# Performance work log

Hardware: AMD Instinct MI355X
Metric: run time of the kernel (lower is better)

The kernel has to match this reference:

```python
import jax, jax.numpy as jnp
import numpy as np

NB, H = 4, 16
EPS = 1e-5


def _ln(x, w=None, b=None):
    m = jnp.mean(x, -1, keepdims=True)
    v = jnp.var(x, -1, keepdims=True)
    y = (x - m) * jax.lax.rsqrt(v + EPS)
    if w is not None:
        y = y * w
    if b is not None:
        y = y + b
    return y


def _ada_ln(a, s, ln_s_w, w_gamma, w_beta):
    # AF3 Algorithm 26: a <- sigmoid(Lin(LN_nobias(s))) * LN_noaffine(a) + Lin(LN_nobias(s))
    a_n = _ln(a)
    s_n = _ln(s, ln_s_w)
    return jax.nn.sigmoid(s_n @ w_gamma) * a_n + s_n @ w_beta


def setup_inputs():
    key = jax.random.key(0)
    B, S, c_a, c_s, c_z = 1, 1024, 768, 384, 128
    n_hidden = 2 * c_a  # expansion factor n=2
    ks = iter(jax.random.split(key, 40))

    def rn(shape, scale=1.0):
        return scale * jax.random.normal(next(ks), shape, dtype=jnp.float32)

    p = 0.02
    return {
        "a": rn((B, S, c_a)),
        "s": rn((B, S, c_s)),
        "z": rn((B, S, S, c_z)),
        "beta": rn((B, S, S, H)),
        # per-block AttentionPairBias params (stacked over NB blocks)
        "ln_s_w_attn": jnp.ones((NB, c_s)),
        "wg_attn": rn((NB, c_s, c_a), p),
        "wb_attn": rn((NB, c_s, c_a), p),
        "wq": rn((NB, c_a, c_a), p),
        "bq": jnp.zeros((NB, c_a)),
        "wk": rn((NB, c_a, c_a), p),
        "wv": rn((NB, c_a, c_a), p),
        "ln_z_w": jnp.ones((NB, c_z)),
        "ln_z_b": jnp.zeros((NB, c_z)),
        "wpb": rn((NB, c_z, H), p),
        "wgate": rn((NB, c_a, c_a), p),
        "wo": rn((NB, c_a, c_a), p),
        "wsg_attn": rn((NB, c_s, c_a), p),
        "bsg_attn": -2.0 * jnp.ones((NB, c_a)),
        # per-block ConditionedTransitionBlock params
        "ln_s_w_tr": jnp.ones((NB, c_s)),
        "wg_tr": rn((NB, c_s, c_a), p),
        "wb_tr": rn((NB, c_s, c_a), p),
        "w_swish": rn((NB, c_a, n_hidden), p),
        "w_gate2": rn((NB, c_a, n_hidden), p),
        "wsg_tr": rn((NB, c_s, c_a), p),
        "bsg_tr": -2.0 * jnp.ones((NB, c_a)),
        "w_out": rn((NB, n_hidden, c_a), p),
    }


def reference(a, s, z, beta, ln_s_w_attn, wg_attn, wb_attn, wq, bq, wk, wv,
              ln_z_w, ln_z_b, wpb, wgate, wo, wsg_attn, bsg_attn,
              ln_s_w_tr, wg_tr, wb_tr, w_swish, w_gate2, wsg_tr, bsg_tr, w_out):
    B, S, c_a = a.shape
    d = c_a // H
    scale = 1.0 / jnp.sqrt(jnp.float32(d))
    for i in range(NB):
        # --- AttentionPairBias (AF3 Alg 24) ---
        ah = _ada_ln(a, s, ln_s_w_attn[i], wg_attn[i], wb_attn[i])
        q = (ah @ wq[i] + bq[i]).reshape(B, S, H, d)
        k = (ah @ wk[i]).reshape(B, S, H, d)
        v = (ah @ wv[i]).reshape(B, S, H, d)
        zb = _ln(z, ln_z_w[i], ln_z_b[i]) @ wpb[i]  # [B,S,S,H] pair bias
        scores = jnp.einsum('bihd,bjhd->bhij', q, k) * scale \
                 + jnp.transpose(zb + beta, (0, 3, 1, 2))
        attn = jax.nn.softmax(scores, axis=-1)
        o = jnp.einsum('bhij,bjhd->bihd', attn, v)
        g = jax.nn.sigmoid(ah @ wgate[i]).reshape(B, S, H, d)
        att_out = (g * o).reshape(B, S, c_a) @ wo[i]
        b_attn = jax.nn.sigmoid(s @ wsg_attn[i] + bsg_attn[i]) * att_out
        # --- ConditionedTransitionBlock (AF3 Alg 25, SwiGLU) ---
        th = _ada_ln(a, s, ln_s_w_tr[i], wg_tr[i], wb_tr[i])
        hidden = jax.nn.silu(th @ w_swish[i]) * (th @ w_gate2[i])
        tr = jax.nn.sigmoid(s @ wsg_tr[i] + bsg_tr[i]) * (hidden @ w_out[i])
        a = b_attn + tr
    return a
```

## Files before the change

### kernel.cpp

```cpp
#include <hip/hip_runtime.h>
#include <hip/hip_bf16.h>

typedef __hip_bfloat16 bf16;
typedef __attribute__((ext_vector_type(8))) short s8v;
typedef __attribute__((ext_vector_type(4))) float f4v;

constexpr int S = 1024, CA = 768, CS = 384, CZ = 128, NHID = 1536;
constexpr int NBLK = 4, NHEAD = 16, DH = 48;
constexpr float EPS = 1e-5f;

#define DEV static __device__ __forceinline__

DEV float sigmoidf_(float x) { return 1.0f / (1.0f + __expf(-x)); }

DEV f4v mfma16(s8v a, s8v b, f4v c) {
  return __builtin_amdgcn_mfma_f32_16x16x32_bf16(a, b, c, 0, 0, 0);
}

union U8 { s8v s; bf16 h[8]; };
union U4 { uint2 u; bf16 h[4]; };

DEV float wred_sum(float v) {
#pragma unroll
  for (int o = 32; o; o >>= 1) v += __shfl_xor(v, o);
  return v;
}

struct PrepFatArgs {
  const float* tsrc[14];
  bf16* tdst[14];
  const float* tcs[14];
  long tdstZ[14];
  const float *ln_z_w, *ln_z_b, *wpb, *bq, *bsg_a, *bsg_t;
  bf16* W2T; float* bias2; float* biasQKVG; float* biasSG;
  const float* s_in; bf16* s_hat; bf16* s_bf;
};

__global__ __launch_bounds__(256) void prep_fat(PrepFatArgs a) {
  __shared__ __align__(16) float tile[1056];
  const int bid = blockIdx.x, t = threadIdx.x;
  if (bid < 32256) {
    int ti, blk, x, y, K, N;
    if (bid < 6912) {
      const int lb = bid; ti = lb / 1152; const int r2 = lb % 1152;
      blk = r2 / 288; const int rem = r2 % 288; x = rem % 24; y = rem / 24; K = 384; N = 768;
    } else if (bid < 18432) {
      const int lb = bid - 6912; ti = 6 + lb / 2304; const int r2 = lb % 2304;
      blk = r2 / 576; const int rem = r2 % 576; x = rem % 24; y = rem / 24; K = 768; N = 768;
    } else if (bid < 27648) {
      const int lb = bid - 18432; ti = 11 + lb / 4608; const int r2 = lb % 4608;
      blk = r2 / 1152; const int rem = r2 % 1152; x = rem % 48; y = rem / 48; K = 768; N = 1536;
    } else {
      const int lb = bid - 27648; ti = 13; blk = lb / 1152;
      const int rem = lb % 1152; x = rem % 24; y = rem / 24; K = 1536; N = 768;
    }
    const float* src = a.tsrc[ti] + (size_t)blk * K * N;
    bf16* dst = a.tdst[ti] + (size_t)blk * a.tdstZ[ti];
    const float* cs = a.tcs[ti] ? (a.tcs[ti] + blk * CS) : nullptr;
    const int k0 = y * 32, n0 = x * 32, tx = t & 31, ty = t >> 5;
#pragma unroll
    for (int q = 0; q < 4; ++q) {
      const int k = k0 + ty + 8 * q;
      float v = src[(size_t)k * N + n0 + tx];
      if (cs) v *= cs[k];
      tile[(ty + 8 * q) * 33 + tx] = v;
    }
    __syncthreads();
#pragma unroll
    for (int q = 0; q < 4; ++q)
      dst[(size_t)(n0 + ty + 8 * q) * K + k0 + tx] = __float2bfloat16(tile[tx * 33 + ty + 8 * q]);
    return;
  }
  if (bid < 32305) {
    const int pid = bid - 32256;
    if (pid == 48) {
      for (int f = t; f < 64 * CZ; f += 256) {
        const int col = f >> 7, c = f & 127, b = col >> 4, h = col & 15;
        a.W2T[f] = __float2bfloat16(a.ln_z_w[b * CZ + c] * a.wpb[(b * CZ + c) * NHEAD + h]);
      }
      if (t < 64) {
        const int b = t >> 4, h = t & 15;
        float sum = 0.f;
        for (int c = 0; c < CZ; ++c)
          sum += a.ln_z_b[b * CZ + c] * a.wpb[(b * CZ + c) * NHEAD + h];
        a.bias2[t] = sum;
      }
      return;
    }
    const int g = pid * 256 + t;
    if (g < 4 * 3072) {
      const int b = g / 3072, c = g % 3072;
      a.biasQKVG[g] = (c < 768) ? a.bq[b * 768 + c] : 0.f;
    }
    if (g < 6144) {
      const int b = g / 1536, c = g % 1536;
      a.biasSG[g] = (c < 768) ? a.bsg_a[b * 768 + c] : a.bsg_t[b * 768 + c - 768];
    }
    return;
  }
  {
    float* red = tile;
    const size_t row = bid - 32305;
    float4 v = make_float4(0.f, 0.f, 0.f, 0.f);
    if (t < CS / 4) v = ((const float4*)(a.s_in + row * CS))[t];
    float sum = v.x + v.y + v.z + v.w;
    float sq = v.x * v.x + v.y * v.y + v.z * v.z + v.w * v.w;
    sum = wred_sum(sum); sq = wred_sum(sq);
    const int wv = t >> 6;
    if ((t & 63) == 0) { red[2 * wv] = sum; red[2 * wv + 1] = sq; }
    __syncthreads();
    sum = red[0] + red[2] + red[4] + red[6];
    sq = red[1] + red[3] + red[5] + red[7];
    const float m = sum / CS;
    const float rstd = rsqrtf(sq / CS - m * m + EPS);
    if (t < CS / 4) {
      U4 oh, ob_;
      oh.h[0] = __float2bfloat16((v.x - m) * rstd); oh.h[1] = __float2bfloat16((v.y - m) * rstd);
      oh.h[2] = __float2bfloat16((v.z - m) * rstd); oh.h[3] = __float2bfloat16((v.w - m) * rstd);
      ob_.h[0] = __float2bfloat16(v.x); ob_.h[1] = __float2bfloat16(v.y);
      ob_.h[2] = __float2bfloat16(v.z); ob_.h[3] = __float2bfloat16(v.w);
      *(uint2*)(a.s_hat + row * CS + 4 * t) = oh.u;
      *(uint2*)(a.s_bf + row * CS + 4 * t) = ob_.u;
    }
  }
}

__global__ __launch_bounds__(256) void ln_adaln2(const float* __restrict__ a,
                                                 const bf16* __restrict__ ada,
                                                 bf16* __restrict__ ah_attn,
                                                 bf16* __restrict__ ah_tr) {
  __shared__ float red[8];
  const int t = threadIdx.x;
  const size_t row = blockIdx.x;
  float4 v = make_float4(0.f, 0.f, 0.f, 0.f);
  if (t < 192) v = ((const float4*)(a + row * CA))[t];
  float sum = v.x + v.y + v.z + v.w;
  float sq = v.x * v.x + v.y * v.y + v.z * v.z + v.w * v.w;
  sum = wred_sum(sum); sq = wred_sum(sq);
  const int wv = t >> 6;
  if ((t & 63) == 0) { red[2 * wv] = sum; red[2 * wv + 1] = sq; }
  __syncthreads();
  sum = red[0] + red[2] + red[4] + red[6];
  sq = red[1] + red[3] + red[5] + red[7];
  const float m = sum / CA;
  const float rstd = rsqrtf(sq / CA - m * m + EPS);
  if (t < 192) {
    const float an[4] = {(v.x - m) * rstd, (v.y - m) * rstd, (v.z - m) * rstd, (v.w - m) * rstd};
    const bf16* ar = ada + row * 12288 + 4 * t;
    U4 g1, b1, g2, b2, o1, o2;
    g1.u = *(const uint2*)(ar);
    b1.u = *(const uint2*)(ar + 768);
    g2.u = *(const uint2*)(ar + 1536);
    b2.u = *(const uint2*)(ar + 2304);
#pragma unroll
    for (int j = 0; j < 4; ++j) {
      o1.h[j] = __float2bfloat16(sigmoidf_(__bfloat162float(g1.h[j])) * an[j] + __bfloat162float(b1.h[j]));
      o2.h[j] = __float2bfloat16(sigmoidf_(__bfloat162float(g2.h[j])) * an[j] + __bfloat162float(b2.h[j]));
    }
    *(uint2*)(ah_attn + row * CA + 4 * t) = o1.u;
    *(uint2*)(ah_tr + row * CA + 4 * t) = o2.u;
  }
}

__global__ __launch_bounds__(256) void final_adaln(const float* __restrict__ sg,
                                                   const bf16* __restrict__ att,
                                                   const bf16* __restrict__ tr,
                                                   const bf16* __restrict__ ada,
                                                   bf16* __restrict__ ah_attn,
                                                   bf16* __restrict__ ah_tr) {
  __shared__ float red[8];
  const int t = threadIdx.x;
  const size_t row = blockIdx.x;
  float o[4] = {0.f, 0.f, 0.f, 0.f};
  if (t < 192) {
    const float4 sa = *(const float4*)(sg + row * 6144 + 4 * t);
    const float4 st = *(const float4*)(sg + row * 6144 + 768 + 4 * t);
    U4 av, tv;
    av.u = *(const uint2*)(att + row * CA + 4 * t);
    tv.u = *(const uint2*)(tr + row * CA + 4 * t);
    o[0] = sa.x * __bfloat162float(av.h[0]) + st.x * __bfloat162float(tv.h[0]);
    o[1] = sa.y * __bfloat162float(av.h[1]) + st.y * __bfloat162float(tv.h[1]);
    o[2] = sa.z * __bfloat162float(av.h[2]) + st.z * __bfloat162float(tv.h[2]);
    o[3] = sa.w * __bfloat162float(av.h[3]) + st.w * __bfloat162float(tv.h[3]);
  }
  float sum = o[0] + o[1] + o[2] + o[3];
  float sq = o[0] * o[0] + o[1] * o[1] + o[2] * o[2] + o[3] * o[3];
  sum = wred_sum(sum); sq = wred_sum(sq);
  const int wv = t >> 6;
  if ((t & 63) == 0) { red[2 * wv] = sum; red[2 * wv + 1] = sq; }
  __syncthreads();
  sum = red[0] + red[2] + red[4] + red[6];
  sq = red[1] + red[3] + red[5] + red[7];
  const float m = sum / CA;
  const float rstd = rsqrtf(sq / CA - m * m + EPS);
  if (t < 192) {
    const bf16* ar = ada + row * 12288 + 4 * t;
    U4 g1, b1, g2, b2, o1, o2;
    g1.u = *(const uint2*)(ar);
    b1.u = *(const uint2*)(ar + 768);
    g2.u = *(const uint2*)(ar + 1536);
    b2.u = *(const uint2*)(ar + 2304);
#pragma unroll
    for (int j = 0; j < 4; ++j) {
      const float an = (o[j] - m) * rstd;
      o1.h[j] = __float2bfloat16(sigmoidf_(__bfloat162float(g1.h[j])) * an + __bfloat162float(b1.h[j]));
      o2.h[j] = __float2bfloat16(sigmoidf_(__bfloat162float(g2.h[j])) * an + __bfloat162float(b2.h[j]));
    }
    *(uint2*)(ah_attn + row * CA + 4 * t) = o1.u;
    *(uint2*)(ah_tr + row * CA + 4 * t) = o2.u;
  }
}

__global__ __launch_bounds__(256) void ew_final(const float* __restrict__ sg,
                                                const bf16* __restrict__ att,
                                                const bf16* __restrict__ tr,
                                                float* __restrict__ out) {
  const int i = blockIdx.x * 256 + threadIdx.x;
  const int row = i / 192, col = (i % 192) * 4;
  const float4 sa = *(const float4*)(sg + (size_t)row * 6144 + col);
  const float4 st = *(const float4*)(sg + (size_t)row * 6144 + 768 + col);
  U4 av, tv;
  av.u = *(const uint2*)(att + (size_t)row * CA + col);
  tv.u = *(const uint2*)(tr + (size_t)row * CA + col);
  float4 o;
  o.x = sa.x * __bfloat162float(av.h[0]) + st.x * __bfloat162float(tv.h[0]);
  o.y = sa.y * __bfloat162float(av.h[1]) + st.y * __bfloat162float(tv.h[1]);
  o.z = sa.z * __bfloat162float(av.h[2]) + st.z * __bfloat162float(tv.h[2]);
  o.w = sa.w * __bfloat162float(av.h[3]) + st.w * __bfloat162float(tv.h[3]);
  *(float4*)(out + (size_t)row * CA + col) = o;
}

__global__ __launch_bounds__(256) void zbias_kernel(const float* __restrict__ z,
                                                    const float* __restrict__ beta,
                                                    const bf16* __restrict__ W2T,
                                                    const float* __restrict__ bias2,
                                                    bf16* __restrict__ bias_all) {
  __shared__ s8v zt8[64 * 16];
  __shared__ s8v w2s[64 * 16];
  __shared__ float betas[64][17];
  __shared__ float bias2s[64];
  __shared__ bf16 obuf[64][72];
  const int t = threadIdx.x;
  const int i = blockIdx.y, j0 = blockIdx.x * 64;
#pragma unroll
  for (int q = 0; q < 4; ++q) {
    const int u = q * 256 + t;
    const int row = u >> 4, sl = u & 15;
    w2s[row * 16 + (sl ^ (row & 7))] = *(const s8v*)(W2T + row * CZ + sl * 8);
  }
  if (t < 64) bias2s[t] = bias2[t];
  {
    const int j = t >> 2, h4 = t & 3;
    const float4 bv = *(const float4*)(beta + ((size_t)i * S + j0 + j) * NHEAD + 4 * h4);
    betas[j][4 * h4 + 0] = bv.x; betas[j][4 * h4 + 1] = bv.y;
    betas[j][4 * h4 + 2] = bv.z; betas[j][4 * h4 + 3] = bv.w;
  }
  {
    const int p = t >> 2, q = t & 3;
    const float* zr = z + ((size_t)i * S + j0 + p) * CZ + q * 32;
    float vals[32];
    float sum = 0.f, sq = 0.f;
#pragma unroll
    for (int k4 = 0; k4 < 8; ++k4) {
      const float4 xv = *(const float4*)(zr + 4 * k4);
      vals[4 * k4 + 0] = xv.x; vals[4 * k4 + 1] = xv.y;
      vals[4 * k4 + 2] = xv.z; vals[4 * k4 + 3] = xv.w;
      sum += xv.x + xv.y + xv.z + xv.w;
      sq += xv.x * xv.x + xv.y * xv.y + xv.z * xv.z + xv.w * xv.w;
    }
    sum += __shfl_xor(sum, 1); sum += __shfl_xor(sum, 2);
    sq += __shfl_xor(sq, 1); sq += __shfl_xor(sq, 2);
    const float m = sum / CZ;
    const float rstd = rsqrtf(sq / CZ - m * m + EPS);
#pragma unroll
    for (int u = 0; u < 4; ++u) {
      U8 pk;
#pragma unroll
      for (int e = 0; e < 8; ++e) pk.h[e] = __float2bfloat16((vals[8 * u + e] - m) * rstd);
      const int cu = 4 * q + u;
      zt8[p * 16 + (cu ^ (p & 7))] = pk.s;
    }
  }
  __syncthreads();
  const int lane = t & 63, wid = t >> 6;
  const int wr = wid >> 1, wc = wid & 1;
  const int ln = lane & 15, lq = lane >> 4;
  f4v acc[2][2] = {};
#pragma unroll
  for (int kk = 0; kk < 4; ++kk) {
    const int sl = (lq + 4 * kk) ^ (ln & 7);
    s8v a[2], b[2];
#pragma unroll
    for (int mi = 0; mi < 2; ++mi) a[mi] = zt8[(32 * wr + 16 * mi + ln) * 16 + sl];
#pragma unroll
    for (int ni = 0; ni < 2; ++ni) b[ni] = w2s[(32 * wc + 16 * ni + ln) * 16 + sl];
#pragma unroll
    for (int mi = 0; mi < 2; ++mi)
#pragma unroll
      for (int ni = 0; ni < 2; ++ni) acc[mi][ni] = mfma16(a[mi], b[ni], acc[mi][ni]);
  }
#pragma unroll
  for (int mi = 0; mi < 2; ++mi)
#pragma unroll
    for (int ni = 0; ni < 2; ++ni) {
      const int col = 32 * wc + 16 * ni + ln;
      const int jb = 32 * wr + 16 * mi + 4 * lq;
      U4 o4;
#pragma unroll
      for (int r = 0; r < 4; ++r)
        o4.h[r] = __float2bfloat16(acc[mi][ni][r] + bias2s[col] + betas[jb + r][col & 15]);
      *(uint2*)&obuf[col][jb] = o4.u;
    }
  __syncthreads();
  {
    const int oc = t >> 2, js = (t & 3) * 16;
    bf16* dp = bias_all + (size_t)oc * S * S + (size_t)i * S + j0 + js;
    *(s8v*)dp = *(const s8v*)&obuf[oc][js];
    *(s8v*)(dp + 8) = *(const s8v*)&obuf[oc][js + 8];
  }
}

struct GemmAArgs {
  const bf16* A0[2]; int lda0[2];
  const bf16* A1[2]; int lda1[2];
  const bf16* Bt[2];
  const float* bias[2];
  void* C[2];
  int K[2]; int N[2]; int nb[2];
  int amode[2]; int outMode[2];
  bf16* vT;
  const float* opA;
  const float* mlA;
  const bf16* gateA;
};

DEV s8v combineRT(s8v x, s8v y, int amode) {
  U8 ux, uy, rr;
  ux.s = x; uy.s = y;
#pragma unroll
  for (int j = 0; j < 8; ++j) {
    const float fx = __bfloat162float(ux.h[j]);
    const float fy = __bfloat162float(uy.h[j]);
    const float tt = sigmoidf_(fx);
    rr.h[j] = __float2bfloat16((amode == 2 ? fx * tt : tt) * fy);
  }
  return rr.s;
}

DEV s8v combineFlash(const float* opart, const float* ml, const bf16* gate,
                     int row, int k) {
  const int h = k / DH;
  const float2 m1 = ((const float2*)ml)[(size_t)h * S + row];
  const float2 m2 = ((const float2*)ml)[(size_t)(NHEAD + h) * S + row];
  const float M = fmaxf(m1.x, m2.x);
  const float w1 = __expf(m1.x - M), w2 = __expf(m2.x - M);
  const float inv = 1.0f / (w1 * m1.y + w2 * m2.y);
  const float* o1p = opart + (size_t)row * CA + k;
  const float* o2p = opart + (size_t)S * CA + (size_t)row * CA + k;
  U8 g; g.s = *(const s8v*)(gate + (size_t)row * 3072 + k);
  U8 r;
#pragma unroll
  for (int j = 0; j < 8; ++j) {
    const float v = (w1 * o1p[j] + w2 * o2p[j]) * inv;
    r.h[j] = __float2bfloat16(sigmoidf_(__bfloat162float(g.h[j])) * v);
  }
  return r.s;
}

__global__ __launch_bounds__(256) void gemmA(GemmAArgs ga) {
  const int z = blockIdx.z;
  if ((int)blockIdx.x >= ga.nb[z]) return;
  __shared__ s8v As[512];
  __shared__ s8v Bs[1024];
  const bf16* A0 = ga.A0[z]; const int lda0 = ga.lda0[z];
  const bf16* A1 = ga.A1[z]; const int lda1 = ga.lda1[z];
  const bf16* Bt = ga.Bt[z];
  const float* bias = ga.bias[z];
  const int K = ga.K[z], N = ga.N[z], amode = ga.amode[z], om = ga.outMode[z];
  const int t = threadIdx.x;
  const int lane = t & 63, wid = t >> 6;
  const int wr = wid >> 1, wc = wid & 1;
  const int ln = lane & 15, lq = lane >> 4;
  const int m0 = blockIdx.y * 64, n0 = blockIdx.x * 128;
  int rowA[2], slA[2], swzA[2];
#pragma unroll
  for (int q = 0; q < 2; ++q) {
    const int u = q * 256 + t;
    rowA[q] = u >> 3; slA[q] = u & 7;
    swzA[q] = rowA[q] * 8 + (slA[q] ^ (rowA[q] & 7));
  }
  int rowB[4], slB[4], swzB[4];
#pragma unroll
  for (int q = 0; q < 4; ++q) {
    const int u = q * 256 + t;
    rowB[q] = u >> 3; slB[q] = u & 7;
    swzB[q] = rowB[q] * 8 + (slB[q] ^ (rowB[q] & 7));
  }
  f4v acc[2][4] = {};
  s8v ra[2], ra2[2], rb[4];
  if (amode != 3) {
#pragma unroll
    for (int q = 0; q < 2; ++q) {
      ra[q] = *(const s8v*)(A0 + (size_t)(m0 + rowA[q]) * lda0 + slA[q] * 8);
      if (amode != 0) ra2[q] = *(const s8v*)(A1 + (size_t)(m0 + rowA[q]) * lda1 + slA[q] * 8);
    }
  }
#pragma unroll
  for (int q = 0; q < 4; ++q)
    rb[q] = *(const s8v*)(Bt + (size_t)(n0 + rowB[q]) * K + slB[q] * 8);
  for (int ks = 0;;) {
    __syncthreads();
    if (amode == 3) {
#pragma unroll
      for (int q = 0; q < 2; ++q)
        As[swzA[q]] = combineFlash(ga.opA, ga.mlA, ga.gateA, m0 + rowA[q], ks + slA[q] * 8);
    } else {
#pragma unroll
      for (int q = 0; q < 2; ++q)
        As[swzA[q]] = (amode == 0) ? ra[q] : combineRT(ra[q], ra2[q], amode);
    }
#pragma unroll
    for (int q = 0; q < 4; ++q) Bs[swzB[q]] = rb[q];
    const int ksn = ks + 64;
    if (ksn < K) {
      if (amode != 3) {
#pragma unroll
        for (int q = 0; q < 2; ++q) {
          ra[q] = *(const s8v*)(A0 + (size_t)(m0 + rowA[q]) * lda0 + ksn + slA[q] * 8);
          if (amode != 0) ra2[q] = *(const s8v*)(A1 + (size_t)(m0 + rowA[q]) * lda1 + ksn + slA[q] * 8);
        }
      }
#pragma unroll
      for (int q = 0; q < 4; ++q)
        rb[q] = *(const s8v*)(Bt + (size_t)(n0 + rowB[q]) * K + ksn + slB[q] * 8);
    }
    __syncthreads();
#pragma unroll
    for (int kk = 0; kk < 2; ++kk) {
      const int sl = (lq + 4 * kk) ^ (ln & 7);
      s8v a[2], b[4];
#pragma unroll
      for (int mi = 0; mi < 2; ++mi) a[mi] = As[(32 * wr + 16 * mi + ln) * 8 + sl];
#pragma unroll
      for (int ni = 0; ni < 4; ++ni) b[ni] = Bs[(64 * wc + 16 * ni + ln) * 8 + sl];
#pragma unroll
      for (int mi = 0; mi < 2; ++mi)
#pragma unroll
        for (int ni = 0; ni < 4; ++ni) acc[mi][ni] = mfma16(a[mi], b[ni], acc[mi][ni]);
    }
    ks = ksn;
    if (ks >= K) break;
  }
  const bool vdiv = (ga.vT != nullptr) && (z == 0) && (n0 >= 1536) && (n0 < 2304);
#pragma unroll
  for (int ni = 0; ni < 4; ++ni) {
    const int n = n0 + 64 * wc + 16 * ni + ln;
    const float bv = bias ? bias[n] : 0.f;
#pragma unroll
    for (int mi = 0; mi < 2; ++mi) {
      const int mb = m0 + 32 * wr + 16 * mi + 4 * lq;
      if (vdiv) {
        U4 o4;
#pragma unroll
        for (int r = 0; r < 4; ++r) o4.h[r] = __float2bfloat16(acc[mi][ni][r] + bv);
        *(uint2*)(ga.vT + (size_t)(n - 1536) * S + mb) = o4.u;
      } else if (om == 0) {
        bf16* Cb = (bf16*)ga.C[z];
#pragma unroll
        for (int r = 0; r < 4; ++r)
          Cb[(size_t)(mb + r) * N + n] = __float2bfloat16(acc[mi][ni][r] + bv);
      } else {
        float* Cf = (float*)ga.C[z];
#pragma unroll
        for (int r = 0; r < 4; ++r)
          Cf[(size_t)(mb + r) * N + n] = sigmoidf_(acc[mi][ni][r] + bv);
      }
    }
  }
}

__global__ __launch_bounds__(256) void flash_split(const bf16* __restrict__ qkvg,
                                                   const bf16* __restrict__ vT,
                                                   const bf16* __restrict__ bias_all,
                                                   float* __restrict__ opart,
                                                   float* __restrict__ ml, int blk) {
  __shared__ s8v Qs[64 * 8];
  __shared__ s8v Ks[2][64 * 8];
  __shared__ s8v Vs[2][48 * 8];
  __shared__ s8v Bs[2][64 * 8];
  __shared__ bf16 PwB[4 * 1024];
  __shared__ float facL[4][16];
  const int t = threadIdx.x;
  const int lane = t & 63, w = t >> 6;
  const int ln = lane & 15, lq = lane >> 4;
  const int h = blockIdx.y, i0 = blockIdx.x * 64, half = blockIdx.z;
  const bf16* bp = bias_all + (size_t)(blk * NHEAD + h) * S * S;
  const float scale = 0.14433756729740643f;

#pragma unroll
  for (int uu = 0; uu < 2; ++uu) {
    const int u = t + 256 * uu, row = u >> 3, sl = u & 7;
    s8v qv{};
    if (sl < 6) qv = *(const s8v*)(qkvg + (size_t)(i0 + row) * 3072 + h * DH + sl * 8);
    Qs[row * 8 + (sl ^ (row & 7))] = qv;
  }

  s8v kr[2], br[2], vr0{}, vr1{};
  auto prefetch = [&](int jt) {
    const int j0 = jt * 64;
#pragma unroll
    for (int uu = 0; uu < 2; ++uu) {
      const int u = t + 256 * uu, row = u >> 3, sl = u & 7;
      s8v kv{};
      if (sl < 6) kv = *(const s8v*)(qkvg + (size_t)(j0 + row) * 3072 + 768 + h * DH + sl * 8);
      kr[uu] = kv;
      br[uu] = *(const s8v*)(bp + (size_t)(i0 + row) * S + j0 + sl * 8);
    }
    { const int d = t >> 3, sl = t & 7;
      vr0 = *(const s8v*)(vT + (size_t)(h * DH + d) * S + j0 + sl * 8); }
    if (t < 128) {
      const int u = 256 + t, d = u >> 3, sl = u & 7;
      vr1 = *(const s8v*)(vT + (size_t)(h * DH + d) * S + j0 + sl * 8);
    }
  };
  auto store_tiles = [&](int pb) {
#pragma unroll
    for (int uu = 0; uu < 2; ++uu) {
      const int u = t + 256 * uu, row = u >> 3, sl = u & 7;
      const int ph = row * 8 + (sl ^ (row & 7));
      Ks[pb][ph] = kr[uu];
      Bs[pb][ph] = br[uu];
    }
    { const int d = t >> 3, sl = t & 7;
      Vs[pb][d * 8 + (sl ^ (d & 7))] = vr0; }
    if (t < 128) {
      const int u = 256 + t, d = u >> 3, sl = u & 7;
      Vs[pb][d * 8 + (sl ^ (d & 7))] = vr1;
    }
  };

  float m_run = -3e30f, l_run = 0.f;
  f4v acc_o[3] = {};
  bf16* pw = PwB + w * 1024;

  prefetch(half * 8);
  for (int jt2 = 0; jt2 < 8; ++jt2) {
    const int pb = jt2 & 1;
    __syncthreads();
    store_tiles(pb);
    __syncthreads();
    if (jt2 < 7) prefetch(half * 8 + jt2 + 1);
    float p[4][4];
    float tmax = -3e30f;
    __builtin_amdgcn_s_setprio(1);
#pragma unroll
    for (int ja = 0; ja < 4; ++ja) {
      f4v accs = {};
#pragma unroll
      for (int ks2 = 0; ks2 < 2; ++ks2) {
        const int sl = (lq + 4 * ks2) ^ (ln & 7);
        const s8v a = Ks[pb][(16 * ja + ln) * 8 + sl];
        const s8v b = Qs[(16 * w + ln) * 8 + sl];
        accs = mfma16(a, b, accs);
      }
      const int jq = 4 * ja + lq;
      const int pu = jq >> 1;
      U4 bv;
      bv.u = *(const uint2*)((const bf16*)(&Bs[pb][0]) +
                             (((16 * w + ln) * 8 + (pu ^ (ln & 7))) * 8 + (jq & 1) * 4));
#pragma unroll
      for (int r = 0; r < 4; ++r) {
        p[ja][r] = accs[r] * scale + __bfloat162float(bv.h[r]);
        tmax = fmaxf(tmax, p[ja][r]);
      }
    }
    __builtin_amdgcn_s_setprio(0);
    tmax = fmaxf(tmax, __shfl_xor(tmax, 16));
    tmax = fmaxf(tmax, __shfl_xor(tmax, 32));
    const float m_new = fmaxf(m_run, tmax);
    const float fac = __expf(m_run - m_new);
    m_run = m_new;
    float psum = 0.f;
#pragma unroll
    for (int ja = 0; ja < 4; ++ja)
#pragma unroll
      for (int r = 0; r < 4; ++r) {
        p[ja][r] = __expf(p[ja][r] - m_new);
        psum += p[ja][r];
      }
    psum += __shfl_xor(psum, 16);
    psum += __shfl_xor(psum, 32);
    l_run = l_run * fac + psum;
    if (lq == 0) facL[w][ln] = fac;
#pragma unroll
    for (int ja = 0; ja < 4; ++ja) {
      const int ju = 4 * ja + lq;
      const int ph = ju ^ ((ln & 7) << 1);
      U4 pk;
#pragma unroll
      for (int r = 0; r < 4; ++r) pk.h[r] = __float2bfloat16(p[ja][r]);
      *(uint2*)(pw + ln * 64 + ph * 4) = pk.u;
    }
    asm volatile("s_waitcnt lgkmcnt(0)" ::: "memory");
    __builtin_amdgcn_sched_barrier(0);
    const float4 fv = *(const float4*)&facL[w][4 * lq];
#pragma unroll
    for (int ni = 0; ni < 3; ++ni) {
      acc_o[ni][0] *= fv.x; acc_o[ni][1] *= fv.y;
      acc_o[ni][2] *= fv.z; acc_o[ni][3] *= fv.w;
    }
    __builtin_amdgcn_s_setprio(1);
#pragma unroll
    for (int ks2 = 0; ks2 < 2; ++ks2) {
      const int pu0 = (2 * lq + 8 * ks2) ^ ((ln & 7) << 1);
      const s8v pa = *(const s8v*)(pw + ln * 64 + pu0 * 4);
      const int slv = (lq + 4 * ks2) ^ (ln & 7);
#pragma unroll
      for (int ni = 0; ni < 3; ++ni) {
        const s8v vb = Vs[pb][(16 * ni + ln) * 8 + slv];
        acc_o[ni] = mfma16(pa, vb, acc_o[ni]);
      }
    }
    __builtin_amdgcn_s_setprio(0);
  }
  if (lq == 0) {
    ((float2*)ml)[(size_t)(half * NHEAD + h) * S + i0 + 16 * w + ln] =
        make_float2(m_run, l_run);
  }
  float* op = opart + (size_t)half * S * CA;
#pragma unroll
  for (int ni = 0; ni < 3; ++ni)
#pragma unroll
    for (int r = 0; r < 4; ++r) {
      const int m = i0 + 16 * w + 4 * lq + r;
      op[(size_t)m * CA + h * DH + 16 * ni + ln] = acc_o[ni][r];
    }
}

__global__ void fill_kernel(float* p, int n, float v) {
  const int i = blockIdx.x * 256 + threadIdx.x;
  if (i < n) p[i] = v;
}

extern "C" void kernel_launch(void* const* d_in, const int* in_sizes, int n_in,
                              void* d_out, int out_size, void* d_ws, size_t ws_size,
                              hipStream_t stream) {
  (void)in_sizes; (void)n_in;
  const float* a_in = (const float*)d_in[0];
  const float* s_in = (const float*)d_in[1];
  const float* z_in = (const float*)d_in[2];
  const float* beta = (const float*)d_in[3];
  const float* ln_s_w_attn = (const float*)d_in[4];
  const float* wg_attn = (const float*)d_in[5];
  const float* wb_attn = (const float*)d_in[6];
  const float* wq = (const float*)d_in[7];
  const float* bq = (const float*)d_in[8];
  const float* wk = (const float*)d_in[9];
  const float* wv = (const float*)d_in[10];
  const float* ln_z_w = (const float*)d_in[11];
  const float* ln_z_b = (const float*)d_in[12];
  const float* wpb = (const float*)d_in[13];
  const float* wgate = (const float*)d_in[14];
  const float* wo = (const float*)d_in[15];
  const float* wsg_attn = (const float*)d_in[16];
  const float* bsg_attn = (const float*)d_in[17];
  const float* ln_s_w_tr = (const float*)d_in[18];
  const float* wg_tr = (const float*)d_in[19];
  const float* wb_tr = (const float*)d_in[20];
  const float* w_swish = (const float*)d_in[21];
  const float* w_gate2 = (const float*)d_in[22];
  const float* wsg_tr = (const float*)d_in[23];
  const float* bsg_tr = (const float*)d_in[24];
  const float* w_out = (const float*)d_in[25];

  char* wp = (char*)d_ws;
  size_t used = 0;
  auto alloc = [&](size_t bytes) -> void* {
    void* p = wp + used;
    used += (bytes + 255) & ~(size_t)255;
    return p;
  };
  bf16* bias_all = (bf16*)alloc((size_t)64 * S * S * 2);
  bf16* WT_ada = (bf16*)alloc((size_t)4 * 3072 * 384 * 2);
  bf16* WT_sg = (bf16*)alloc((size_t)4 * 1536 * 384 * 2);
  bf16* WT_qkvg = (bf16*)alloc((size_t)4 * 3072 * 768 * 2);
  bf16* WT_wo = (bf16*)alloc((size_t)4 * 768 * 768 * 2);
  bf16* WT_mlp = (bf16*)alloc((size_t)4 * 3072 * 768 * 2);
  bf16* WT_wout = (bf16*)alloc((size_t)4 * 768 * 1536 * 2);
  float* biasQKVG = (float*)alloc(4 * 3072 * 4);
  float* biasSG = (float*)alloc(6144 * 4);
  bf16* W2T = (bf16*)alloc(64 * 128 * 2);
  float* bias2 = (float*)alloc(64 * 4);
  bf16* ada_all = (bf16*)alloc((size_t)S * 12288 * 2);
  float* sg_all = (float*)alloc((size_t)S * 6144 * 4);
  bf16* s_hat = (bf16*)alloc((size_t)S * CS * 2);
  bf16* s_bf = (bf16*)alloc((size_t)S * CS * 2);
  bf16* ah_attn = (bf16*)alloc((size_t)S * CA * 2);
  bf16* ah_tr = (bf16*)alloc((size_t)S * CA * 2);
  bf16* qkvg = (bf16*)alloc((size_t)S * 3072 * 2);
  bf16* vT = (bf16*)alloc((size_t)CA * S * 2);
  bf16* att = (bf16*)alloc((size_t)S * CA * 2);
  bf16* swg = (bf16*)alloc((size_t)S * 3072 * 2);
  bf16* trout = (bf16*)alloc((size_t)S * CA * 2);
  float* opart = (float*)alloc((size_t)2 * S * CA * 4);
  float* ml = (float*)alloc((size_t)2 * NHEAD * S * 8);
  if (used > ws_size) {
    fill_kernel<<<(out_size + 255) / 256, 256, 0, stream>>>((float*)d_out, out_size, 12345.0f);
    return;
  }

  const dim3 B256(256);

  {
    PrepFatArgs pa{};
    pa.tsrc[0] = wg_attn;  pa.tdst[0] = WT_ada + (size_t)0 * 384;    pa.tcs[0] = ln_s_w_attn; pa.tdstZ[0] = 3072 * 384;
    pa.tsrc[1] = wb_attn;  pa.tdst[1] = WT_ada + (size_t)768 * 384;  pa.tcs[1] = ln_s_w_attn; pa.tdstZ[1] = 3072 * 384;
    pa.tsrc[2] = wg_tr;    pa.tdst[2] = WT_ada + (size_t)1536 * 384; pa.tcs[2] = ln_s_w_tr;   pa.tdstZ[2] = 3072 * 384;
    pa.tsrc[3] = wb_tr;    pa.tdst[3] = WT_ada + (size_t)2304 * 384; pa.tcs[3] = ln_s_w_tr;   pa.tdstZ[3] = 3072 * 384;
    pa.tsrc[4] = wsg_attn; pa.tdst[4] = WT_sg + (size_t)0 * 384;     pa.tcs[4] = nullptr;     pa.tdstZ[4] = 1536 * 384;
    pa.tsrc[5] = wsg_tr;   pa.tdst[5] = WT_sg + (size_t)768 * 384;   pa.tcs[5] = nullptr;     pa.tdstZ[5] = 1536 * 384;
    pa.tsrc[6] = wq;    pa.tdst[6] = WT_qkvg + (size_t)0 * 768;    pa.tdstZ[6] = 3072 * 768;
    pa.tsrc[7] = wk;    pa.tdst[7] = WT_qkvg + (size_t)768 * 768;  pa.tdstZ[7] = 3072 * 768;
    pa.tsrc[8] = wv;    pa.tdst[8] = WT_qkvg + (size_t)1536 * 768; pa.tdstZ[8] = 3072 * 768;
    pa.tsrc[9] = wgate; pa.tdst[9] = WT_qkvg + (size_t)2304 * 768; pa.tdstZ[9] = 3072 * 768;
    pa.tsrc[10] = wo;   pa.tdst[10] = WT_wo;                       pa.tdstZ[10] = 768 * 768;
    pa.tsrc[11] = w_swish; pa.tdst[11] = WT_mlp + (size_t)0 * 768;    pa.tdstZ[11] = 3072 * 768;
    pa.tsrc[12] = w_gate2; pa.tdst[12] = WT_mlp + (size_t)1536 * 768; pa.tdstZ[12] = 3072 * 768;
    pa.tsrc[13] = w_out; pa.tdst[13] = WT_wout; pa.tdstZ[13] = 768 * 1536;
    pa.ln_z_w = ln_z_w; pa.ln_z_b = ln_z_b; pa.wpb = wpb;
    pa.bq = bq; pa.bsg_a = bsg_attn; pa.bsg_t = bsg_tr;
    pa.W2T = W2T; pa.bias2 = bias2; pa.biasQKVG = biasQKVG; pa.biasSG = biasSG;
    pa.s_in = s_in; pa.s_hat = s_hat; pa.s_bf = s_bf;
    prep_fat<<<33329, B256, 0, stream>>>(pa);
  }

  zbias_kernel<<<dim3(16, 1024), B256, 0, stream>>>(z_in, beta, W2T, bias2, bias_all);

  {
    GemmAArgs ga{};
    ga.A0[0] = s_hat; ga.lda0[0] = 384; ga.Bt[0] = WT_ada; ga.bias[0] = nullptr;
    ga.C[0] = ada_all; ga.K[0] = 384; ga.N[0] = 12288; ga.nb[0] = 96;
    ga.amode[0] = 0; ga.outMode[0] = 0;
    ga.A0[1] = s_bf; ga.lda0[1] = 384; ga.Bt[1] = WT_sg; ga.bias[1] = biasSG;
    ga.C[1] = sg_all; ga.K[1] = 384; ga.N[1] = 6144; ga.nb[1] = 48;
    ga.amode[1] = 0; ga.outMode[1] = 1;
    ga.vT = nullptr;
    gemmA<<<dim3(96, 16, 2), B256, 0, stream>>>(ga);
  }

  ln_adaln2<<<S, B256, 0, stream>>>(a_in, ada_all, ah_attn, ah_tr);
  for (int b = 0; b < NBLK; ++b) {
    {
      GemmAArgs ga{};
      ga.A0[0] = ah_attn; ga.lda0[0] = 768; ga.Bt[0] = WT_qkvg + (size_t)b * 3072 * 768;
      ga.bias[0] = biasQKVG + b * 3072; ga.C[0] = qkvg; ga.K[0] = 768; ga.N[0] = 3072;
      ga.nb[0] = 24; ga.amode[0] = 0; ga.outMode[0] = 0;
      ga.A0[1] = ah_tr; ga.lda0[1] = 768; ga.Bt[1] = WT_mlp + (size_t)b * 3072 * 768;
      ga.bias[1] = nullptr; ga.C[1] = swg; ga.K[1] = 768; ga.N[1] = 3072;
      ga.nb[1] = 24; ga.amode[1] = 0; ga.outMode[1] = 0;
      ga.vT = vT;
      gemmA<<<dim3(24, 16, 2), B256, 0, stream>>>(ga);
    }
    flash_split<<<dim3(16, 16, 2), B256, 0, stream>>>(qkvg, vT, bias_all, opart, ml, b);
    {
      GemmAArgs ga{};
      ga.A0[0] = nullptr; ga.lda0[0] = 0;
      ga.Bt[0] = WT_wo + (size_t)b * 768 * 768; ga.bias[0] = nullptr;
      ga.C[0] = att; ga.K[0] = 768; ga.N[0] = 768; ga.nb[0] = 6;
      ga.amode[0] = 3; ga.outMode[0] = 0;
      ga.A0[1] = swg; ga.lda0[1] = 3072; ga.A1[1] = swg + 1536; ga.lda1[1] = 3072;
      ga.Bt[1] = WT_wout + (size_t)b * 768 * 1536; ga.bias[1] = nullptr;
      ga.C[1] = trout; ga.K[1] = 1536; ga.N[1] = 768; ga.nb[1] = 6;
      ga.amode[1] = 2; ga.outMode[1] = 0;
      ga.vT = nullptr;
      ga.opA = opart; ga.mlA = ml; ga.gateA = qkvg + 2304;
      gemmA<<<dim3(6, 16, 2), B256, 0, stream>>>(ga);
    }
    if (b < NBLK - 1) {
      final_adaln<<<S, B256, 0, stream>>>(sg_all + (size_t)b * 1536, att, trout,
                                          ada_all + (size_t)(b + 1) * 3072, ah_attn, ah_tr);
    } else {
      ew_final<<<768, B256, 0, stream>>>(sg_all + (size_t)b * 1536, att, trout, (float*)d_out);
    }
  }
}
```

Before: 542.3 us.

## Fuse attention-out and transition-out GEMMs with gated residual into one tail kernel

Replaces the two-branch gemmA launch (Wo projection and W_out projection written to bf16 buffers) plus the final_adaln/ew_final combine with a single gemm_tail kernel. Each block computes both GEMMs into separate accumulators over 64x64 tiles and applies the sigmoid gates in the epilogue, writing the fp32 residual directly. The next block's adaLN then reuses ln_adaln2 on that fp32 buffer. This removes the att/trout intermediate round trips and one launch per block, and keeps the pre-LN sum in fp32. In exchange, gemm_tail uses smaller tiles with no register prefetch, and each block runs a sequential K=768 loop followed by a K=1536 loop, which may reduce latency hiding and per-block efficiency.

```diff
diff --git a/kernel.cpp b/kernel.cpp
--- a/kernel.cpp
+++ b/kernel.cpp
@@ -162,74 +162,6 @@
   }
 }
 
-__global__ __launch_bounds__(256) void final_adaln(const float* __restrict__ sg,
-                                                   const bf16* __restrict__ att,
-                                                   const bf16* __restrict__ tr,
-                                                   const bf16* __restrict__ ada,
-                                                   bf16* __restrict__ ah_attn,
-                                                   bf16* __restrict__ ah_tr) {
-  __shared__ float red[8];
-  const int t = threadIdx.x;
-  const size_t row = blockIdx.x;
-  float o[4] = {0.f, 0.f, 0.f, 0.f};
-  if (t < 192) {
-    const float4 sa = *(const float4*)(sg + row * 6144 + 4 * t);
-    const float4 st = *(const float4*)(sg + row * 6144 + 768 + 4 * t);
-    U4 av, tv;
-    av.u = *(const uint2*)(att + row * CA + 4 * t);
-    tv.u = *(const uint2*)(tr + row * CA + 4 * t);
-    o[0] = sa.x * __bfloat162float(av.h[0]) + st.x * __bfloat162float(tv.h[0]);
-    o[1] = sa.y * __bfloat162float(av.h[1]) + st.y * __bfloat162float(tv.h[1]);
-    o[2] = sa.z * __bfloat162float(av.h[2]) + st.z * __bfloat162float(tv.h[2]);
-    o[3] = sa.w * __bfloat162float(av.h[3]) + st.w * __bfloat162float(tv.h[3]);
-  }
-  float sum = o[0] + o[1] + o[2] + o[3];
-  float sq = o[0] * o[0] + o[1] * o[1] + o[2] * o[2] + o[3] * o[3];
-  sum = wred_sum(sum); sq = wred_sum(sq);
-  const int wv = t >> 6;
-  if ((t & 63) == 0) { red[2 * wv] = sum; red[2 * wv + 1] = sq; }
-  __syncthreads();
-  sum = red[0] + red[2] + red[4] + red[6];
-  sq = red[1] + red[3] + red[5] + red[7];
-  const float m = sum / CA;
-  const float rstd = rsqrtf(sq / CA - m * m + EPS);
-  if (t < 192) {
-    const bf16* ar = ada + row * 12288 + 4 * t;
-    U4 g1, b1, g2, b2, o1, o2;
-    g1.u = *(const uint2*)(ar);
-    b1.u = *(const uint2*)(ar + 768);
-    g2.u = *(const uint2*)(ar + 1536);
-    b2.u = *(const uint2*)(ar + 2304);
-#pragma unroll
-    for (int j = 0; j < 4; ++j) {
-      const float an = (o[j] - m) * rstd;
-      o1.h[j] = __float2bfloat16(sigmoidf_(__bfloat162float(g1.h[j])) * an + __bfloat162float(b1.h[j]));
-      o2.h[j] = __float2bfloat16(sigmoidf_(__bfloat162float(g2.h[j])) * an + __bfloat162float(b2.h[j]));
-    }
-    *(uint2*)(ah_attn + row * CA + 4 * t) = o1.u;
-    *(uint2*)(ah_tr + row * CA + 4 * t) = o2.u;
-  }
-}
-
-__global__ __launch_bounds__(256) void ew_final(const float* __restrict__ sg,
-                                                const bf16* __restrict__ att,
-                                                const bf16* __restrict__ tr,
-                                                float* __restrict__ out) {
-  const int i = blockIdx.x * 256 + threadIdx.x;
-  const int row = i / 192, col = (i % 192) * 4;
-  const float4 sa = *(const float4*)(sg + (size_t)row * 6144 + col);
-  const float4 st = *(const float4*)(sg + (size_t)row * 6144 + 768 + col);
-  U4 av, tv;
-  av.u = *(const uint2*)(att + (size_t)row * CA + col);
-  tv.u = *(const uint2*)(tr + (size_t)row * CA + col);
-  float4 o;
-  o.x = sa.x * __bfloat162float(av.h[0]) + st.x * __bfloat162float(tv.h[0]);
-  o.y = sa.y * __bfloat162float(av.h[1]) + st.y * __bfloat162float(tv.h[1]);
-  o.z = sa.z * __bfloat162float(av.h[2]) + st.z * __bfloat162float(tv.h[2]);
-  o.w = sa.w * __bfloat162float(av.h[3]) + st.w * __bfloat162float(tv.h[3]);
-  *(float4*)(out + (size_t)row * CA + col) = o;
-}
-
 __global__ __launch_bounds__(256) void zbias_kernel(const float* __restrict__ z,
                                                     const float* __restrict__ beta,
                                                     const bf16* __restrict__ W2T,
@@ -320,20 +252,6 @@
   }
 }
 
-struct GemmAArgs {
-  const bf16* A0[2]; int lda0[2];
-  const bf16* A1[2]; int lda1[2];
-  const bf16* Bt[2];
-  const float* bias[2];
-  void* C[2];
-  int K[2]; int N[2]; int nb[2];
-  int amode[2]; int outMode[2];
-  bf16* vT;
-  const float* opA;
-  const float* mlA;
-  const bf16* gateA;
-};
-
 DEV s8v combineRT(s8v x, s8v y, int amode) {
   U8 ux, uy, rr;
   ux.s = x; uy.s = y;
@@ -367,16 +285,25 @@
   return r.s;
 }
 
+struct GemmAArgs {
+  const bf16* A0[2]; int lda0[2];
+  const bf16* Bt[2];
+  const float* bias[2];
+  void* C[2];
+  int K[2]; int N[2]; int nb[2];
+  int outMode[2];
+  bf16* vT;
+};
+
 __global__ __launch_bounds__(256) void gemmA(GemmAArgs ga) {
   const int z = blockIdx.z;
   if ((int)blockIdx.x >= ga.nb[z]) return;
   __shared__ s8v As[512];
   __shared__ s8v Bs[1024];
   const bf16* A0 = ga.A0[z]; const int lda0 = ga.lda0[z];
-  const bf16* A1 = ga.A1[z]; const int lda1 = ga.lda1[z];
   const bf16* Bt = ga.Bt[z];
   const float* bias = ga.bias[z];
-  const int K = ga.K[z], N = ga.N[z], amode = ga.amode[z], om = ga.outMode[z];
+  const int K = ga.K[z], N = ga.N[z], om = ga.outMode[z];
   const int t = threadIdx.x;
   const int lane = t & 63, wid = t >> 6;
   const int wr = wid >> 1, wc = wid & 1;
@@ -397,39 +324,24 @@
     swzB[q] = rowB[q] * 8 + (slB[q] ^ (rowB[q] & 7));
   }
   f4v acc[2][4] = {};
-  s8v ra[2], ra2[2], rb[4];
-  if (amode != 3) {
-#pragma unroll
-    for (int q = 0; q < 2; ++q) {
-      ra[q] = *(const s8v*)(A0 + (size_t)(m0 + rowA[q]) * lda0 + slA[q] * 8);
-      if (amode != 0) ra2[q] = *(const s8v*)(A1 + (size_t)(m0 + rowA[q]) * lda1 + slA[q] * 8);
-    }
-  }
+  s8v ra[2], rb[4];
+#pragma unroll
+  for (int q = 0; q < 2; ++q)
+    ra[q] = *(const s8v*)(A0 + (size_t)(m0 + rowA[q]) * lda0 + slA[q] * 8);
 #pragma unroll
   for (int q = 0; q < 4; ++q)
     rb[q] = *(const s8v*)(Bt + (size_t)(n0 + rowB[q]) * K + slB[q] * 8);
   for (int ks = 0;;) {
     __syncthreads();
-    if (amode == 3) {
-#pragma unroll
-      for (int q = 0; q < 2; ++q)
-        As[swzA[q]] = combineFlash(ga.opA, ga.mlA, ga.gateA, m0 + rowA[q], ks + slA[q] * 8);
-    } else {
-#pragma unroll
-      for (int q = 0; q < 2; ++q)
-        As[swzA[q]] = (amode == 0) ? ra[q] : combineRT(ra[q], ra2[q], amode);
-    }
+#pragma unroll
+    for (int q = 0; q < 2; ++q) As[swzA[q]] = ra[q];
 #pragma unroll
     for (int q = 0; q < 4; ++q) Bs[swzB[q]] = rb[q];
     const int ksn = ks + 64;
     if (ksn < K) {
-      if (amode != 3) {
-#pragma unroll
-        for (int q = 0; q < 2; ++q) {
-          ra[q] = *(const s8v*)(A0 + (size_t)(m0 + rowA[q]) * lda0 + ksn + slA[q] * 8);
-          if (amode != 0) ra2[q] = *(const s8v*)(A1 + (size_t)(m0 + rowA[q]) * lda1 + ksn + slA[q] * 8);
-        }
-      }
+#pragma unroll
+      for (int q = 0; q < 2; ++q)
+        ra[q] = *(const s8v*)(A0 + (size_t)(m0 + rowA[q]) * lda0 + ksn + slA[q] * 8);
 #pragma unroll
       for (int q = 0; q < 4; ++q)
         rb[q] = *(const s8v*)(Bt + (size_t)(n0 + rowB[q]) * K + ksn + slB[q] * 8);
@@ -474,6 +386,93 @@
 #pragma unroll
         for (int r = 0; r < 4; ++r)
           Cf[(size_t)(mb + r) * N + n] = sigmoidf_(acc[mi][ni][r] + bv);
+      }
+    }
+  }
+}
+
+struct GemmTailArgs {
+  const float* opA; const float* mlA; const bf16* gateA;
+  const bf16* swg;
+  const bf16* BtWo; const bf16* BtWout;
+  const float* sg;
+  float* out;
+};
+
+__global__ __launch_bounds__(256) void gemm_tail(GemmTailArgs ga) {
+  __shared__ s8v As[512];
+  __shared__ s8v Bs[512];
+  const int t = threadIdx.x;
+  const int lane = t & 63, wid = t >> 6;
+  const int wr = wid >> 1, wc = wid & 1;
+  const int ln = lane & 15, lq = lane >> 4;
+  const int m0 = blockIdx.y * 64, n0 = blockIdx.x * 64;
+  int rowS[2], slS[2], swz[2];
+#pragma unroll
+  for (int q = 0; q < 2; ++q) {
+    const int u = q * 256 + t;
+    rowS[q] = u >> 3; slS[q] = u & 7;
+    swz[q] = rowS[q] * 8 + (slS[q] ^ (rowS[q] & 7));
+  }
+  f4v acc1[2][2] = {}, acc2[2][2] = {};
+  for (int ks = 0; ks < 768; ks += 64) {
+    __syncthreads();
+#pragma unroll
+    for (int q = 0; q < 2; ++q) {
+      As[swz[q]] = combineFlash(ga.opA, ga.mlA, ga.gateA, m0 + rowS[q], ks + slS[q] * 8);
+      Bs[swz[q]] = *(const s8v*)(ga.BtWo + (size_t)(n0 + rowS[q]) * 768 + ks + slS[q] * 8);
+    }
+    __syncthreads();
+#pragma unroll
+    for (int kk = 0; kk < 2; ++kk) {
+      const int sl = (lq + 4 * kk) ^ (ln & 7);
+      s8v a[2], b[2];
+#pragma unroll
+      for (int mi = 0; mi < 2; ++mi) a[mi] = As[(32 * wr + 16 * mi + ln) * 8 + sl];
+#pragma unroll
+      for (int ni = 0; ni < 2; ++ni) b[ni] = Bs[(32 * wc + 16 * ni + ln) * 8 + sl];
+#pragma unroll
+      for (int mi = 0; mi < 2; ++mi)
+#pragma unroll
+        for (int ni = 0; ni < 2; ++ni) acc1[mi][ni] = mfma16(a[mi], b[ni], acc1[mi][ni]);
+    }
+  }
+  for (int ks = 0; ks < 1536; ks += 64) {
+    __syncthreads();
+#pragma unroll
+    for (int q = 0; q < 2; ++q) {
+      const s8v x = *(const s8v*)(ga.swg + (size_t)(m0 + rowS[q]) * 3072 + ks + slS[q] * 8);
+      const s8v y = *(const s8v*)(ga.swg + (size_t)(m0 + rowS[q]) * 3072 + 1536 + ks + slS[q] * 8);
+      As[swz[q]] = combineRT(x, y, 2);
+      Bs[swz[q]] = *(const s8v*)(ga.BtWout + (size_t)(n0 + rowS[q]) * 1536 + ks + slS[q] * 8);
+    }
+    __syncthreads();
+#pragma unroll
+    for (int kk = 0; kk < 2; ++kk) {
+      const int sl = (lq + 4 * kk) ^ (ln & 7);
+      s8v a[2], b[2];
+#pragma unroll
+      for (int mi = 0; mi < 2; ++mi) a[mi] = As[(32 * wr + 16 * mi + ln) * 8 + sl];
+#pragma unroll
+      for (int ni = 0; ni < 2; ++ni) b[ni] = Bs[(32 * wc + 16 * ni + ln) * 8 + sl];
+#pragma unroll
+      for (int mi = 0; mi < 2; ++mi)
+#pragma unroll
+        for (int ni = 0; ni < 2; ++ni) acc2[mi][ni] = mfma16(a[mi], b[ni], acc2[mi][ni]);
+    }
+  }
+#pragma unroll
+  for (int ni = 0; ni < 2; ++ni) {
+    const int n = n0 + 32 * wc + 16 * ni + ln;
+#pragma unroll
+    for (int mi = 0; mi < 2; ++mi) {
+      const int mb = m0 + 32 * wr + 16 * mi + 4 * lq;
+#pragma unroll
+      for (int r = 0; r < 4; ++r) {
+        const int row = mb + r;
+        const float sgA = ga.sg[(size_t)row * 6144 + n];
+        const float sgT = ga.sg[(size_t)row * 6144 + 768 + n];
+        ga.out[(size_t)row * CA + n] = sgA * acc1[mi][ni][r] + sgT * acc2[mi][ni][r];
       }
     }
   }
@@ -695,13 +694,12 @@
   float* sg_all = (float*)alloc((size_t)S * 6144 * 4);
   bf16* s_hat = (bf16*)alloc((size_t)S * CS * 2);
   bf16* s_bf = (bf16*)alloc((size_t)S * CS * 2);
+  float* a_buf = (float*)alloc((size_t)S * CA * 4);
   bf16* ah_attn = (bf16*)alloc((size_t)S * CA * 2);
   bf16* ah_tr = (bf16*)alloc((size_t)S * CA * 2);
   bf16* qkvg = (bf16*)alloc((size_t)S * 3072 * 2);
   bf16* vT = (bf16*)alloc((size_t)CA * S * 2);
-  bf16* att = (bf16*)alloc((size_t)S * CA * 2);
   bf16* swg = (bf16*)alloc((size_t)S * 3072 * 2);
-  bf16* trout = (bf16*)alloc((size_t)S * CA * 2);
   float* opart = (float*)alloc((size_t)2 * S * CA * 4);
   float* ml = (float*)alloc((size_t)2 * NHEAD * S * 8);
   if (used > ws_size) {
@@ -739,11 +737,9 @@
   {
     GemmAArgs ga{};
     ga.A0[0] = s_hat; ga.lda0[0] = 384; ga.Bt[0] = WT_ada; ga.bias[0] = nullptr;
-    ga.C[0] = ada_all; ga.K[0] = 384; ga.N[0] = 12288; ga.nb[0] = 96;
-    ga.amode[0] = 0; ga.outMode[0] = 0;
+    ga.C[0] = ada_all; ga.K[0] = 384; ga.N[0] = 12288; ga.nb[0] = 96; ga.outMode[0] = 0;
     ga.A0[1] = s_bf; ga.lda0[1] = 384; ga.Bt[1] = WT_sg; ga.bias[1] = biasSG;
-    ga.C[1] = sg_all; ga.K[1] = 384; ga.N[1] = 6144; ga.nb[1] = 48;
-    ga.amode[1] = 0; ga.outMode[1] = 1;
+    ga.C[1] = sg_all; ga.K[1] = 384; ga.N[1] = 6144; ga.nb[1] = 48; ga.outMode[1] = 1;
     ga.vT = nullptr;
     gemmA<<<dim3(96, 16, 2), B256, 0, stream>>>(ga);
   }
@@ -754,33 +750,26 @@
       GemmAArgs ga{};
       ga.A0[0] = ah_attn; ga.lda0[0] = 768; ga.Bt[0] = WT_qkvg + (size_t)b * 3072 * 768;
       ga.bias[0] = biasQKVG + b * 3072; ga.C[0] = qkvg; ga.K[0] = 768; ga.N[0] = 3072;
-      ga.nb[0] = 24; ga.amode[0] = 0; ga.outMode[0] = 0;
+      ga.nb[0] = 24; ga.outMode[0] = 0;
       ga.A0[1] = ah_tr; ga.lda0[1] = 768; ga.Bt[1] = WT_mlp + (size_t)b * 3072 * 768;
       ga.bias[1] = nullptr; ga.C[1] = swg; ga.K[1] = 768; ga.N[1] = 3072;
-      ga.nb[1] = 24; ga.amode[1] = 0; ga.outMode[1] = 0;
+      ga.nb[1] = 24; ga.outMode[1] = 0;
       ga.vT = vT;
       gemmA<<<dim3(24, 16, 2), B256, 0, stream>>>(ga);
     }
     flash_split<<<dim3(16, 16, 2), B256, 0, stream>>>(qkvg, vT, bias_all, opart, ml, b);
+    float* a_next = (b == NBLK - 1) ? (float*)d_out : a_buf;
     {
-      GemmAArgs ga{};
-      ga.A0[0] = nullptr; ga.lda0[0] = 0;
-      ga.Bt[0] = WT_wo + (size_t)b * 768 * 768; ga.bias[0] = nullptr;
-      ga.C[0] = att; ga.K[0] = 768; ga.N[0] = 768; ga.nb[0] = 6;
-      ga.amode[0] = 3; ga.outMode[0] = 0;
-      ga.A0[1] = swg; ga.lda0[1] = 3072; ga.A1[1] = swg + 1536; ga.lda1[1] = 3072;
-      ga.Bt[1] = WT_wout + (size_t)b * 768 * 1536; ga.bias[1] = nullptr;
-      ga.C[1] = trout; ga.K[1] = 1536; ga.N[1] = 768; ga.nb[1] = 6;
-      ga.amode[1] = 2; ga.outMode[1] = 0;
-      ga.vT = nullptr;
-      ga.opA = opart; ga.mlA = ml; ga.gateA = qkvg + 2304;
-      gemmA<<<dim3(6, 16, 2), B256, 0, stream>>>(ga);
-    }
-    if (b < NBLK - 1) {
-      final_adaln<<<S, B256, 0, stream>>>(sg_all + (size_t)b * 1536, att, trout,
-                                          ada_all + (size_t)(b + 1) * 3072, ah_attn, ah_tr);
-    } else {
-      ew_final<<<768, B256, 0, stream>>>(sg_all + (size_t)b * 1536, att, trout, (float*)d_out);
-    }
-  }
-}
+      GemmTailArgs ta{};
+      ta.opA = opart; ta.mlA = ml; ta.gateA = qkvg + 2304;
+      ta.swg = swg;
+      ta.BtWo = WT_wo + (size_t)b * 768 * 768;
+      ta.BtWout = WT_wout + (size_t)b * 768 * 1536;
+      ta.sg = sg_all + (size_t)b * 1536;
+      ta.out = a_next;
+      gemm_tail<<<dim3(12, 16), B256, 0, stream>>>(ta);
+    }
+    if (b < NBLK - 1)
+      ln_adaln2<<<S, B256, 0, stream>>>(a_next, ada_all + (size_t)(b + 1) * 3072, ah_attn, ah_tr);
+  }
+}
```

Result: slower. 789.7 us (+45.6%).
